# Kernel optimization log

Measured on AMD Instinct MI355X. Metric: run time of the kernel, lower is better.

The kernel has to match this reference:

```python
import jax, jax.numpy as jnp
import numpy as np

N, E = 20000, 320000
H1, C1 = 8, 128   # gat1 heads/out
H2, C2 = 1, 128   # gat2 heads/out
D_IN = 768
NEG_SLOPE = 0.2
BN_EPS = 1e-5


def setup_inputs() -> dict:
    key = jax.random.key(0)
    ks = jax.random.split(key, 16)
    def rn(k, shape, fan):
        return jax.random.normal(k, shape, dtype=jnp.float32) / np.sqrt(fan)
    x = jax.random.normal(ks[0], (N, D_IN), dtype=jnp.float32)
    edge_index = jax.random.randint(ks[1], (2, E), 0, N, dtype=jnp.int64)
    return {
        "x": x,
        "edge_index": edge_index,
        "W1": rn(ks[2], (D_IN, H1 * C1), D_IN),
        "att_src1": rn(ks[3], (H1, C1), C1),
        "att_dst1": rn(ks[4], (H1, C1), C1),
        "b1": jnp.zeros((H1 * C1,), jnp.float32),
        "W2": rn(ks[5], (H1 * C1, H2 * C2), H1 * C1),
        "att_src2": rn(ks[6], (H2, C2), C2),
        "att_dst2": rn(ks[7], (H2, C2), C2),
        "b2": jnp.zeros((C2,), jnp.float32),
        "g1": jnp.ones((H1 * C1,), jnp.float32),
        "be1": jnp.zeros((H1 * C1,), jnp.float32),
        "g2": jnp.ones((C2,), jnp.float32),
        "be2": jnp.zeros((C2,), jnp.float32),
        "Wc1": rn(ks[8], (C2, 64), C2),
        "bc1": jnp.zeros((64,), jnp.float32),
        "Wc2": rn(ks[9], (64, 2), 64),
        "bc2": jnp.zeros((2,), jnp.float32),
    }


def gat_conv(x, src, dst, W, att_src, att_dst, bias, heads, ch, concat):
    n = x.shape[0]
    h = (x @ W).reshape(n, heads, ch)                      # [N,H,C]
    a_s = jnp.sum(h * att_src[None], axis=-1)              # [N,H]
    a_d = jnp.sum(h * att_dst[None], axis=-1)
    e = a_s[src] + a_d[dst]                                # [Et,H]
    e = jax.nn.leaky_relu(e, NEG_SLOPE)
    # segment softmax over incoming edges of each dst node
    m = jax.ops.segment_max(e, dst, num_segments=n)
    ex = jnp.exp(e - m[dst])
    z = jax.ops.segment_sum(ex, dst, num_segments=n)
    alpha = ex / z[dst]                                    # [Et,H]
    msg = alpha[:, :, None] * h[src]                       # [Et,H,C]
    out = jax.ops.segment_sum(msg, dst, num_segments=n)    # [N,H,C]
    if concat:
        out = out.reshape(n, heads * ch)
    else:
        out = out.mean(axis=1)
    return out + bias


def batch_norm(x, gamma, beta):
    mu = x.mean(axis=0)
    var = x.var(axis=0)
    return (x - mu) * jax.lax.rsqrt(var + BN_EPS) * gamma + beta


def reference(x, edge_index, W1, att_src1, att_dst1, b1, W2, att_src2, att_dst2, b2,
              g1, be1, g2, be2, Wc1, bc1, Wc2, bc2):
    n = x.shape[0]
    loop = jnp.arange(n, dtype=edge_index.dtype)
    src = jnp.concatenate([edge_index[0], loop])  # PyG add_self_loops default
    dst = jnp.concatenate([edge_index[1], loop])
    h = gat_conv(x, src, dst, W1, att_src1, att_dst1, b1, H1, C1, True)
    h = jax.nn.elu(batch_norm(h, g1, be1))
    h = gat_conv(h, src, dst, W2, att_src2, att_dst2, b2, H2, C2, False)
    h = jax.nn.elu(batch_norm(h, g2, be2))
    h = jax.nn.relu(h @ Wc1 + bc1)
    return h @ Wc2 + bc2
```

## Files before the change

kernel.cpp:

```cpp
#include <hip/hip_runtime.h>
#include <hip/hip_bf16.h>
#include <math.h>

#define N_NODES 20000
#define N_EDGES 320000
#define DIN 768
#define F1 1024
#define H1 8
#define C1 128
#define F2 128
#define NEG_SLOPE 0.2f
#define BN_EPS 1e-5f
#define RESCALE_THR 8.0f

typedef __attribute__((ext_vector_type(8))) __bf16 bf16x8;
typedef __attribute__((ext_vector_type(4))) float f32x4;

__device__ __forceinline__ float leaky(float x) { return x > 0.f ? x : NEG_SLOPE * x; }

__device__ __forceinline__ unsigned short f2bu(float x) {
  __hip_bfloat16 b = __float2bfloat16(x);
  return *(unsigned short*)&b;
}
__device__ __forceinline__ float b2f(unsigned short u) {
  return __uint_as_float(((unsigned)u) << 16);
}
__device__ __forceinline__ unsigned pack2(float lo, float hi) {
  return (unsigned)f2bu(lo) | ((unsigned)f2bu(hi) << 16);
}

__device__ __forceinline__ void async_copy16(void* lds, const void* g) {
  __builtin_amdgcn_global_load_lds(
      (const __attribute__((address_space(1))) unsigned int*)g,
      (__attribute__((address_space(3))) unsigned int*)lds, 16, 0, 0);
}

__global__ void repack_hist_kernel(const int* raw, int* ei32, int* deg) {
  int is64 = (raw[1] == 0 && raw[3] == 0 && raw[5] == 0 && raw[7] == 0) ? 1 : 0;
  int e = blockIdx.x * blockDim.x + threadIdx.x;
  if (e < 2 * N_EDGES) {
    int v = is64 ? raw[2 * e] : raw[e];
    ei32[e] = v;
    if (e >= N_EDGES) atomicAdd(&deg[v], 1);
  }
}

#define NPT 20
__global__ __launch_bounds__(1024) void scan_kernel(const int* __restrict__ deg,
                                                    int* __restrict__ off,
                                                    int* __restrict__ cursor) {
  __shared__ int wsum[16];
  int tid = threadIdx.x;
  int lane = tid & 63, wv = tid >> 6;
  int base = tid * NPT;
  int loc[NPT];
  int run = 0;
#pragma unroll
  for (int k = 0; k < NPT; ++k) {
    int i = base + k;
    int v = (i < N_NODES) ? deg[i] : 0;
    loc[k] = run;
    run += v;
  }
  int incl = run;
  for (int sh = 1; sh < 64; sh <<= 1) {
    int t = __shfl_up(incl, sh, 64);
    if (lane >= sh) incl += t;
  }
  if (lane == 63) wsum[wv] = incl;
  __syncthreads();
  if (wv == 0 && lane < 16) {
    int v = wsum[lane];
    for (int sh = 1; sh < 16; sh <<= 1) {
      int t = __shfl_up(v, sh, 16);
      if (lane >= sh) v += t;
    }
    wsum[lane] = v;
  }
  __syncthreads();
  int wbase = (wv > 0) ? wsum[wv - 1] : 0;
  int tbase = wbase + incl - run;
#pragma unroll
  for (int k = 0; k < NPT; ++k) {
    int i = base + k;
    if (i < N_NODES) {
      int o = tbase + loc[k];
      off[i] = o;
      cursor[i] = o;
    }
  }
  if (tid == 1023) off[N_NODES] = wbase + incl;
}

__global__ void scatter_kernel(const int* ei, int* cursor, int* elist) {
  int e = blockIdx.x * blockDim.x + threadIdx.x;
  if (e < N_EDGES) {
    int dst = ei[N_EDGES + e];
    int p = atomicAdd(&cursor[dst], 1);
    elist[p] = ei[e];
  }
}

__global__ void f2b_kernel(const float* __restrict__ in, unsigned short* __restrict__ out,
                           size_t n4) {
  size_t i = (size_t)blockIdx.x * blockDim.x + threadIdx.x;
  size_t stride = (size_t)gridDim.x * blockDim.x;
  for (; i < n4; i += stride) {
    float4 v = ((const float4*)in)[i];
    ushort4 u;
    u.x = f2bu(v.x); u.y = f2bu(v.y); u.z = f2bu(v.z); u.w = f2bu(v.w);
    ((ushort4*)out)[i] = u;
  }
}

__global__ void transpose_b_kernel(const float* __restrict__ W, unsigned short* __restrict__ WT,
                                   int K, int N) {
  __shared__ float t[32][33];
  int k0 = blockIdx.y * 32, n0 = blockIdx.x * 32;
  int tx = threadIdx.x & 31, ty = threadIdx.x >> 5;
  for (int i = 0; i < 32; i += 8)
    t[ty + i][tx] = W[(size_t)(k0 + ty + i) * N + n0 + tx];
  __syncthreads();
  for (int i = 0; i < 32; i += 8)
    WT[(size_t)(n0 + ty + i) * K + k0 + tx] = f2bu(t[tx][ty + i]);
}

#define GBM 128
#define GBN 128
#define GBK 64
template <int H, int SWZ>
__global__ __launch_bounds__(256) void mfma_gemm_att_kernel(
    const unsigned short* __restrict__ A,
    const unsigned short* __restrict__ BT,
    unsigned short* __restrict__ C,
    const float* __restrict__ att_src,
    const float* __restrict__ att_dst,
    float* __restrict__ as_out,
    float* __restrict__ ad_out,
    int M, int N, int K) {
  __shared__ __hip_bfloat16 As[GBM][GBK];
  __shared__ __hip_bfloat16 Bs[GBN][GBK];
  __shared__ float sred[128][2];
  __shared__ float dred[128][2];
  int bx, by;
  if (SWZ) {
    int bid = blockIdx.x;
    int pl = bid & 7, c = (bid >> 3) & 7, ph = bid >> 6;
    int p = ph * 8 + pl;
    if (p * GBM >= M) return;
    by = p; bx = c;
  } else {
    bx = blockIdx.x; by = blockIdx.y;
  }
  int tid = threadIdx.x;
  int lane = tid & 63, wid = tid >> 6;
  int wr = wid >> 1, wc = wid & 1;
  int row0 = by * GBM, col0 = bx * GBN;
  int head = bx;
  int l16 = lane & 15, l4 = lane >> 4;
  f32x4 acc[4][4] = {};
  for (int k0 = 0; k0 < K; k0 += GBK) {
#pragma unroll
    for (int j = 0; j < 4; ++j) {
      int c = j * 256 + tid;
      int r = c >> 3, kk = (c & 7) << 3;
      int ga = row0 + r; if (ga >= M) ga = M - 1;
      async_copy16(&As[r][kk], A + (size_t)ga * K + k0 + kk);
      async_copy16(&Bs[r][kk], BT + (size_t)(col0 + r) * K + k0 + kk);
    }
    __syncthreads();
#pragma unroll
    for (int ks = 0; ks < 2; ++ks) {
      bf16x8 af[4], bfr[4];
#pragma unroll
      for (int i = 0; i < 4; ++i)
        af[i] = *(const bf16x8*)&As[wr * 64 + i * 16 + l16][ks * 32 + l4 * 8];
#pragma unroll
      for (int j = 0; j < 4; ++j)
        bfr[j] = *(const bf16x8*)&Bs[wc * 64 + j * 16 + l16][ks * 32 + l4 * 8];
#pragma unroll
      for (int i = 0; i < 4; ++i)
#pragma unroll
        for (int j = 0; j < 4; ++j)
          acc[i][j] = __builtin_amdgcn_mfma_f32_16x16x32_bf16(af[i], bfr[j], acc[i][j], 0, 0, 0);
    }
    __syncthreads();
  }
#pragma unroll
  for (int i = 0; i < 4; ++i) {
#pragma unroll
    for (int j = 0; j < 4; ++j) {
#pragma unroll
      for (int r = 0; r < 4; ++r) {
        int row = row0 + wr * 64 + i * 16 + l4 * 4 + r;
        int col = col0 + wc * 64 + j * 16 + l16;
        if (row < M) C[(size_t)row * N + col] = f2bu(acc[i][j][r]);
      }
    }
  }
  float avs[4], avd[4];
#pragma unroll
  for (int j = 0; j < 4; ++j) {
    int col = col0 + wc * 64 + j * 16 + l16;
    avs[j] = att_src[col];
    avd[j] = att_dst[col];
  }
#pragma unroll
  for (int i = 0; i < 4; ++i) {
#pragma unroll
    for (int r = 0; r < 4; ++r) {
      float ps = 0.f, pd = 0.f;
#pragma unroll
      for (int j = 0; j < 4; ++j) { ps += acc[i][j][r] * avs[j]; pd += acc[i][j][r] * avd[j]; }
#pragma unroll
      for (int mk = 1; mk < 16; mk <<= 1) {
        ps += __shfl_xor(ps, mk, 64);
        pd += __shfl_xor(pd, mk, 64);
      }
      if (l16 == 0) {
        int lr = wr * 64 + i * 16 + l4 * 4 + r;
        sred[lr][wc] = ps;
        dred[lr][wc] = pd;
      }
    }
  }
  __syncthreads();
  if (tid < 128) {
    int row = row0 + tid;
    if (row < M) {
      as_out[(size_t)row * H + head] = sred[tid][0] + sred[tid][1];
      ad_out[(size_t)row * H + head] = dred[tid][0] + dred[tid][1];
    }
  }
}

__global__ __launch_bounds__(64) void alpha1_kernel(const float* __restrict__ as1,
                                                    const float* __restrict__ ad1,
                                                    const int* __restrict__ off,
                                                    const int* __restrict__ elist,
                                                    uint2* __restrict__ ewT,
                                                    float* __restrict__ zinv,
                                                    float* __restrict__ wself) {
  int node = blockIdx.x;
  int lane = threadIdx.x;
  int s = off[node], e = off[node + 1];
  float4 adlo = *(const float4*)(ad1 + node * H1);
  float4 adhi = *(const float4*)(ad1 + node * H1 + 4);
  float ad[8] = {adlo.x, adlo.y, adlo.z, adlo.w, adhi.x, adhi.y, adhi.z, adhi.w};
  float4 aslo = *(const float4*)(as1 + node * H1);
  float4 ashi = *(const float4*)(as1 + node * H1 + 4);
  float sl[8] = {aslo.x, aslo.y, aslo.z, aslo.w, ashi.x, ashi.y, ashi.z, ashi.w};
  float m[8];
#pragma unroll
  for (int h = 0; h < 8; ++h) { sl[h] = leaky(sl[h] + ad[h]); m[h] = sl[h]; }
  for (int i = s + lane; i < e; i += 64) {
    int src = elist[i];
    float4 lo = *(const float4*)(as1 + (size_t)src * H1);
    float4 hi = *(const float4*)(as1 + (size_t)src * H1 + 4);
    float v[8] = {lo.x, lo.y, lo.z, lo.w, hi.x, hi.y, hi.z, hi.w};
#pragma unroll
    for (int h = 0; h < 8; ++h) m[h] = fmaxf(m[h], leaky(v[h] + ad[h]));
  }
#pragma unroll
  for (int h = 0; h < 8; ++h)
    for (int sh = 32; sh >= 1; sh >>= 1) m[h] = fmaxf(m[h], __shfl_xor(m[h], sh, 64));
  float z[8] = {0.f, 0.f, 0.f, 0.f, 0.f, 0.f, 0.f, 0.f};
  for (int i = s + lane; i < e; i += 64) {
    int src = elist[i];
    float4 lo = *(const float4*)(as1 + (size_t)src * H1);
    float4 hi = *(const float4*)(as1 + (size_t)src * H1 + 4);
    float v[8] = {lo.x, lo.y, lo.z, lo.w, hi.x, hi.y, hi.z, hi.w};
#pragma unroll
    for (int h = 0; h < 8; ++h) {
      float w = __expf(leaky(v[h] + ad[h]) - m[h]);
      z[h] += w;
      ewT[(size_t)h * N_EDGES + i] = make_uint2((unsigned)src, __float_as_uint(w));
    }
  }
#pragma unroll
  for (int h = 0; h < 8; ++h)
    for (int sh = 32; sh >= 1; sh >>= 1) z[h] += __shfl_xor(z[h], sh, 64);
  if (lane == 0) {
#pragma unroll
    for (int h = 0; h < 8; ++h) {
      float ws = __expf(sl[h] - m[h]);
      zinv[node * H1 + h] = 1.f / (z[h] + ws);
      wself[node * H1 + h] = ws;
    }
  }
}

#define EW_LOAD(i, ev)                                                          \
  if ((i) < e) ev = ewp[(i)];
#define H1_LOAD(i, ev, rv)                                                      \
  if ((i) < e) rv = *(const unsigned*)(h1 + (size_t)ev.x * F1 + cb);
#define GW_CONS(u, ev)                                                          \
  {                                                                             \
    float wv = __uint_as_float(ev.y);                                           \
    a0 += wv * __uint_as_float(u << 16);                                        \
    a1 += wv * __uint_as_float(u & 0xffff0000u);                                \
  }

__global__ __launch_bounds__(64) void gatherw1_kernel(const unsigned short* __restrict__ h1,
                                                      const uint2* __restrict__ ewT,
                                                      const float* __restrict__ zinv,
                                                      const float* __restrict__ wself,
                                                      const int* __restrict__ off,
                                                      const float* __restrict__ b1,
                                                      unsigned short* __restrict__ out1) {
  int head = blockIdx.x;
  int node = blockIdx.y;
  int tid = threadIdx.x;
  int cb = head * C1 + tid * 2;
  int s = off[node], e = off[node + 1];
  const uint2* ewp = ewT + (size_t)head * N_EDGES;
  float a0, a1;
  {
    float ws = wself[node * H1 + head];
    unsigned u = *(const unsigned*)(h1 + (size_t)node * F1 + cb);
    a0 = ws * __uint_as_float(u << 16);
    a1 = ws * __uint_as_float(u & 0xffff0000u);
  }
  uint2 ea0 = {0, 0}, ea1 = {0, 0}, ea2 = {0, 0}, ea3 = {0, 0};
  uint2 eb0 = {0, 0}, eb1 = {0, 0}, eb2 = {0, 0}, eb3 = {0, 0};
  unsigned ra0 = 0, ra1 = 0, ra2 = 0, ra3 = 0;
  EW_LOAD(s + 0, ea0)
  EW_LOAD(s + 1, ea1)
  EW_LOAD(s + 2, ea2)
  EW_LOAD(s + 3, ea3)
  EW_LOAD(s + 4, eb0)
  EW_LOAD(s + 5, eb1)
  EW_LOAD(s + 6, eb2)
  EW_LOAD(s + 7, eb3)
  H1_LOAD(s + 0, ea0, ra0)
  H1_LOAD(s + 1, ea1, ra1)
  H1_LOAD(s + 2, ea2, ra2)
  H1_LOAD(s + 3, ea3, ra3)
  for (int base = s; base < e; base += 4) {
    unsigned rb0 = 0, rb1 = 0, rb2 = 0, rb3 = 0;
    int nb = base + 4;
    H1_LOAD(nb + 0, eb0, rb0)
    H1_LOAD(nb + 1, eb1, rb1)
    H1_LOAD(nb + 2, eb2, rb2)
    H1_LOAD(nb + 3, eb3, rb3)
    uint2 ec0 = {0, 0}, ec1 = {0, 0}, ec2 = {0, 0}, ec3 = {0, 0};
    int nc = base + 8;
    EW_LOAD(nc + 0, ec0)
    EW_LOAD(nc + 1, ec1)
    EW_LOAD(nc + 2, ec2)
    EW_LOAD(nc + 3, ec3)
    GW_CONS(ra0, ea0)
    GW_CONS(ra1, ea1)
    GW_CONS(ra2, ea2)
    GW_CONS(ra3, ea3)
    ea0 = eb0; ea1 = eb1; ea2 = eb2; ea3 = eb3;
    eb0 = ec0; eb1 = ec1; eb2 = ec2; eb3 = ec3;
    ra0 = rb0; ra1 = rb1; ra2 = rb2; ra3 = rb3;
  }
  float inv = zinv[node * H1 + head];
  float2 bv = *(const float2*)(b1 + cb);
  unsigned o = pack2(a0 * inv + bv.x, a1 * inv + bv.y);
  *(unsigned*)(out1 + (size_t)node * F1 + cb) = o;
}

__global__ void bnstats_bf16_kernel(const unsigned short* __restrict__ x,
                                    float* __restrict__ sums,
                                    int nrows, int F, int rowsPerBlock) {
  int tid = threadIdx.x;
  int c = tid * 4;
  int r0 = blockIdx.x * rowsPerBlock;
  int rend = min(r0 + rowsPerBlock, nrows);
  float s0 = 0.f, s1 = 0.f, s2 = 0.f, s3 = 0.f;
  float q0 = 0.f, q1 = 0.f, q2 = 0.f, q3 = 0.f;
  for (int r = r0; r < rend; ++r) {
    ushort4 u = *(const ushort4*)(x + (size_t)r * F + c);
    float v0 = b2f(u.x), v1 = b2f(u.y), v2 = b2f(u.z), v3 = b2f(u.w);
    s0 += v0; s1 += v1; s2 += v2; s3 += v3;
    q0 += v0 * v0; q1 += v1 * v1; q2 += v2 * v2; q3 += v3 * v3;
  }
  atomicAdd(&sums[c + 0], s0); atomicAdd(&sums[c + 1], s1);
  atomicAdd(&sums[c + 2], s2); atomicAdd(&sums[c + 3], s3);
  atomicAdd(&sums[F + c + 0], q0); atomicAdd(&sums[F + c + 1], q1);
  atomicAdd(&sums[F + c + 2], q2); atomicAdd(&sums[F + c + 3], q3);
}

template <int CPT>
__global__ void bnstats_kernel(const float* __restrict__ x, float* __restrict__ sums,
                               int nrows, int F, int rowsPerBlock) {
  int tid = threadIdx.x;
  int r0 = blockIdx.x * rowsPerBlock;
  int rend = min(r0 + rowsPerBlock, nrows);
  float s[CPT], q[CPT];
#pragma unroll
  for (int k = 0; k < CPT; ++k) { s[k] = 0.f; q[k] = 0.f; }
  for (int r = r0; r < rend; ++r) {
    const float* row = x + (size_t)r * F;
#pragma unroll
    for (int k = 0; k < CPT; ++k) {
      float v = row[tid + k * blockDim.x];
      s[k] += v; q[k] += v * v;
    }
  }
#pragma unroll
  for (int k = 0; k < CPT; ++k) {
    atomicAdd(&sums[tid + k * blockDim.x], s[k]);
    atomicAdd(&sums[F + tid + k * blockDim.x], q[k]);
  }
}

__global__ void bnfinal_kernel(const float* __restrict__ sums, const float* __restrict__ g,
                               const float* __restrict__ be, float* __restrict__ ss, int F) {
  int c = blockIdx.x * blockDim.x + threadIdx.x;
  if (c < F) {
    float mu = sums[c] * (1.f / N_NODES);
    float var = sums[F + c] * (1.f / N_NODES) - mu * mu;
    float sc = g[c] * rsqrtf(var + BN_EPS);
    ss[c] = sc;
    ss[F + c] = be[c] - mu * sc;
  }
}

__global__ void bnapply_bf16_kernel(unsigned short* __restrict__ x, const float* __restrict__ ss,
                                    int F, size_t total4) {
  size_t i = (size_t)blockIdx.x * blockDim.x + threadIdx.x;
  size_t stride = (size_t)gridDim.x * blockDim.x;
  for (; i < total4; i += stride) {
    int c = (int)((i * 4) & (size_t)(F - 1));
    ushort4 u = ((ushort4*)x)[i];
    float v0 = b2f(u.x) * ss[c + 0] + ss[F + c + 0];
    float v1 = b2f(u.y) * ss[c + 1] + ss[F + c + 1];
    float v2 = b2f(u.z) * ss[c + 2] + ss[F + c + 2];
    float v3 = b2f(u.w) * ss[c + 3] + ss[F + c + 3];
    v0 = v0 > 0.f ? v0 : expm1f(v0);
    v1 = v1 > 0.f ? v1 : expm1f(v1);
    v2 = v2 > 0.f ? v2 : expm1f(v2);
    v3 = v3 > 0.f ? v3 : expm1f(v3);
    u.x = f2bu(v0); u.y = f2bu(v1); u.z = f2bu(v2); u.w = f2bu(v3);
    ((ushort4*)x)[i] = u;
  }
}

#define G2_LOAD(i, rv, ev)                                                     \
  if ((i) < e) {                                                               \
    int ssrc = elist[(i)];                                                     \
    ev = leaky(as2[ssrc] + ad);                                                \
    rv = *(const unsigned*)(h2 + (size_t)ssrc * F2 + tid * 2);                 \
  }
#define G2_CONSUME(u, el)                                                      \
  {                                                                            \
    float w;                                                                   \
    if (el > m + RESCALE_THR) {                                                \
      float rr = __expf(m - el);                                               \
      z *= rr; a0 *= rr; a1 *= rr;                                             \
      m = el; w = 1.f;                                                         \
    } else {                                                                   \
      w = __expf(el - m);                                                      \
    }                                                                          \
    z += w;                                                                    \
    a0 += w * __uint_as_float(u << 16);                                        \
    a1 += w * __uint_as_float(u & 0xffff0000u);                                \
  }

__global__ __launch_bounds__(64) void gather2_kernel(const unsigned short* __restrict__ h2,
                                                     const float* __restrict__ as2,
                                                     const float* __restrict__ ad2,
                                                     const int* __restrict__ off,
                                                     const int* __restrict__ elist,
                                                     const float* __restrict__ b2,
                                                     float* __restrict__ out2) {
  int node = blockIdx.x;
  int tid = threadIdx.x;
  const float ad = ad2[node];
  int s = off[node], e = off[node + 1];
  float m = leaky(as2[node] + ad);
  float z = 1.f;
  float a0, a1;
  {
    unsigned u = *(const unsigned*)(h2 + (size_t)node * F2 + tid * 2);
    a0 = __uint_as_float(u << 16); a1 = __uint_as_float(u & 0xffff0000u);
  }
  unsigned ra0 = 0, ra1 = 0, ra2 = 0, ra3 = 0;
  float ea0 = 0.f, ea1 = 0.f, ea2 = 0.f, ea3 = 0.f;
  G2_LOAD(s + 0, ra0, ea0)
  G2_LOAD(s + 1, ra1, ea1)
  G2_LOAD(s + 2, ra2, ea2)
  G2_LOAD(s + 3, ra3, ea3)
  for (int base = s; base < e; base += 4) {
    unsigned rb0 = 0, rb1 = 0, rb2 = 0, rb3 = 0;
    float eb0 = 0.f, eb1 = 0.f, eb2 = 0.f, eb3 = 0.f;
    int nb = base + 4;
    G2_LOAD(nb + 0, rb0, eb0)
    G2_LOAD(nb + 1, rb1, eb1)
    G2_LOAD(nb + 2, rb2, eb2)
    G2_LOAD(nb + 3, rb3, eb3)
    G2_CONSUME(ra0, ea0)
    if (base + 1 < e) G2_CONSUME(ra1, ea1)
    if (base + 2 < e) G2_CONSUME(ra2, ea2)
    if (base + 3 < e) G2_CONSUME(ra3, ea3)
    ra0 = rb0; ra1 = rb1; ra2 = rb2; ra3 = rb3;
    ea0 = eb0; ea1 = eb1; ea2 = eb2; ea3 = eb3;
  }
  float inv = 1.f / z;
  float2 o = make_float2(a0 * inv + b2[tid * 2 + 0], a1 * inv + b2[tid * 2 + 1]);
  *(float2*)(out2 + (size_t)node * F2 + tid * 2) = o;
}

__global__ __launch_bounds__(64) void cls_kernel(const float* __restrict__ h,
                                                 const float* __restrict__ ss2,
                                                 const float* __restrict__ Wc1,
                                                 const float* __restrict__ bc1,
                                                 const float* __restrict__ Wc2,
                                                 const float* __restrict__ bc2,
                                                 float* __restrict__ out) {
  __shared__ float hl[128];
  int node = blockIdx.x;
  int tid = threadIdx.x;
  {
    float v = h[(size_t)node * F2 + tid] * ss2[tid] + ss2[F2 + tid];
    v = v > 0.f ? v : expm1f(v);
    hl[tid] = v;
    float v2 = h[(size_t)node * F2 + 64 + tid] * ss2[64 + tid] + ss2[F2 + 64 + tid];
    v2 = v2 > 0.f ? v2 : expm1f(v2);
    hl[tid + 64] = v2;
  }
  __syncthreads();
  float acc = bc1[tid];
#pragma unroll
  for (int k = 0; k < 128; ++k) acc += hl[k] * Wc1[k * 64 + tid];
  acc = fmaxf(acc, 0.f);
  float2 w = *(const float2*)(Wc2 + tid * 2);
  float o0 = acc * w.x, o1 = acc * w.y;
  for (int sh = 32; sh >= 1; sh >>= 1) {
    o0 += __shfl_down(o0, sh, 64);
    o1 += __shfl_down(o1, sh, 64);
  }
  if (tid == 0) {
    out[node * 2 + 0] = o0 + bc2[0];
    out[node * 2 + 1] = o1 + bc2[1];
  }
}

extern "C" void kernel_launch(void* const* d_in, const int* in_sizes, int n_in,
                              void* d_out, int out_size, void* d_ws, size_t ws_size,
                              hipStream_t stream) {
  const float* x        = (const float*)d_in[0];
  const int*   ei_raw   = (const int*)d_in[1];
  const float* W1       = (const float*)d_in[2];
  const float* att_src1 = (const float*)d_in[3];
  const float* att_dst1 = (const float*)d_in[4];
  const float* b1       = (const float*)d_in[5];
  const float* W2       = (const float*)d_in[6];
  const float* att_src2 = (const float*)d_in[7];
  const float* att_dst2 = (const float*)d_in[8];
  const float* b2       = (const float*)d_in[9];
  const float* g1       = (const float*)d_in[10];
  const float* be1      = (const float*)d_in[11];
  const float* g2       = (const float*)d_in[12];
  const float* be2      = (const float*)d_in[13];
  const float* Wc1      = (const float*)d_in[14];
  const float* bc1      = (const float*)d_in[15];
  const float* Wc2      = (const float*)d_in[16];
  const float* bc2      = (const float*)d_in[17];
  float* out = (float*)d_out;

  char* ws = (char*)d_ws;
  size_t o = 0;
  unsigned short* h1b   = (unsigned short*)(ws + o); o += (size_t)N_NODES * F1 * 2;
  unsigned short* out1b = (unsigned short*)(ws + o); o += (size_t)N_NODES * F1 * 2;
  unsigned short* xb    = (unsigned short*)(ws + o); o += (size_t)N_NODES * DIN * 2;
  unsigned short* h2b   = (unsigned short*)(ws + o); o += (size_t)N_NODES * F2 * 2;
  float* out2  = (float*)(ws + o); o += (size_t)N_NODES * F2 * 4;
  float* as1   = (float*)(ws + o); o += (size_t)N_NODES * H1 * 4;
  float* ad1   = (float*)(ws + o); o += (size_t)N_NODES * H1 * 4;
  float* as2   = (float*)(ws + o); o += (size_t)N_NODES * 4;
  float* ad2   = (float*)(ws + o); o += (size_t)N_NODES * 4;
  uint2* ewT   = (uint2*)(ws + o); o += (size_t)H1 * N_EDGES * 8;
  float* zinv  = (float*)(ws + o); o += (size_t)N_NODES * H1 * 4;
  float* wself = (float*)(ws + o); o += (size_t)N_NODES * H1 * 4;
  char*  zbase = ws + o;
  float* bnsum1 = (float*)(ws + o); o += F1 * 2 * 4;
  float* bnsum2 = (float*)(ws + o); o += F2 * 2 * 4;
  int*   deg    = (int*)(ws + o); o += (size_t)N_NODES * 4;
  size_t zbytes = (size_t)((ws + o) - zbase);
  int*   offv   = (int*)(ws + o); o += (size_t)(N_NODES + 4) * 4;
  int*   cursor = (int*)(ws + o); o += (size_t)N_NODES * 4;
  int*   elist  = (int*)(ws + o); o += (size_t)N_EDGES * 4;
  float* ss1    = (float*)(ws + o); o += F1 * 2 * 4;
  float* ss2    = (float*)(ws + o); o += F2 * 2 * 4;
  int*   ei32   = (int*)(ws + o); o += (size_t)2 * N_EDGES * 4;
  unsigned short* W1T = (unsigned short*)(ws + o); o += (size_t)F1 * DIN * 2;
  unsigned short* W2T = (unsigned short*)(ws + o); o += (size_t)F2 * F1 * 2;
  (void)ws_size; (void)in_sizes; (void)n_in; (void)out_size;

  hipMemsetAsync((void*)zbase, 0, zbytes, stream);

  f2b_kernel<<<2048, 256, 0, stream>>>(x, xb, (size_t)N_NODES * DIN / 4);
  {
    dim3 g1d(F1 / 32, DIN / 32);
    transpose_b_kernel<<<g1d, 256, 0, stream>>>(W1, W1T, DIN, F1);
    dim3 g2d(F2 / 32, F1 / 32);
    transpose_b_kernel<<<g2d, 256, 0, stream>>>(W2, W2T, F1, F2);
  }

  repack_hist_kernel<<<(2 * N_EDGES + 255) / 256, 256, 0, stream>>>(ei_raw, ei32, deg);
  scan_kernel<<<1, 1024, 0, stream>>>(deg, offv, cursor);
  scatter_kernel<<<(N_EDGES + 255) / 256, 256, 0, stream>>>(ei32, cursor, elist);

  {
    int panels = (N_NODES + GBM - 1) / GBM;
    int grid1 = ((panels + 7) / 8) * 64;
    mfma_gemm_att_kernel<H1, 1><<<grid1, 256, 0, stream>>>(
        xb, W1T, h1b, att_src1, att_dst1, as1, ad1, N_NODES, F1, DIN);
  }
  alpha1_kernel<<<N_NODES, 64, 0, stream>>>(as1, ad1, offv, elist, ewT, zinv, wself);
  gatherw1_kernel<<<dim3(H1, N_NODES), 64, 0, stream>>>(
      h1b, ewT, zinv, wself, offv, b1, out1b);
  {
    int rows = 79;
    int grid = (N_NODES + rows - 1) / rows;
    bnstats_bf16_kernel<<<grid, 256, 0, stream>>>(out1b, bnsum1, N_NODES, F1, rows);
  }
  bnfinal_kernel<<<(F1 + 255) / 256, 256, 0, stream>>>(bnsum1, g1, be1, ss1, F1);
  bnapply_bf16_kernel<<<2048, 256, 0, stream>>>(out1b, ss1, F1, (size_t)N_NODES * F1 / 4);

  {
    dim3 grid(F2 / GBN, (N_NODES + GBM - 1) / GBM);
    mfma_gemm_att_kernel<1, 0><<<grid, 256, 0, stream>>>(
        out1b, W2T, h2b, att_src2, att_dst2, as2, ad2, N_NODES, F2, F1);
  }
  gather2_kernel<<<N_NODES, 64, 0, stream>>>(h2b, as2, ad2, offv, elist, b2, out2);
  {
    int rows = 79;
    int grid = (N_NODES + rows - 1) / rows;
    bnstats_kernel<1><<<grid, 128, 0, stream>>>(out2, bnsum2, N_NODES, F2, rows);
  }
  bnfinal_kernel<<<1, F2, 0, stream>>>(bnsum2, g2, be2, ss2, F2);

  cls_kernel<<<N_NODES, 64, 0, stream>>>(out2, ss2, Wc1, bc1, Wc2, bc2, out);
}
```

Baseline: 447.6 us.

## Split-K second GAT GEMM, two-pass layer-2 softmax, batched classifier, drop edge repack

Several independent changes. The second GEMM (only one 128-column tile) is split along K into two partial fp32 products reduced by a new combine kernel, which doubles the block count. The layer-2 online-softmax gather is replaced by a separate alpha pass plus a prefetching weighted gather, mirroring layer 1. The classifier now processes 16 nodes per 256-thread block with Wc1 cached in LDS. The int64-to-int32 edge repack is removed so hist and scatter read the raw indices directly. The costs are extra fp32 partial traffic and an extra kernel launch.

```diff
diff --git a/kernel.cpp b/kernel.cpp
--- a/kernel.cpp
+++ b/kernel.cpp
@@ -11,7 +11,6 @@
 #define F2 128
 #define NEG_SLOPE 0.2f
 #define BN_EPS 1e-5f
-#define RESCALE_THR 8.0f
 
 typedef __attribute__((ext_vector_type(8))) __bf16 bf16x8;
 typedef __attribute__((ext_vector_type(4))) float f32x4;
@@ -35,13 +34,12 @@
       (__attribute__((address_space(3))) unsigned int*)lds, 16, 0, 0);
 }
 
-__global__ void repack_hist_kernel(const int* raw, int* ei32, int* deg) {
+__global__ void hist_kernel(const int* raw, int* deg) {
   int is64 = (raw[1] == 0 && raw[3] == 0 && raw[5] == 0 && raw[7] == 0) ? 1 : 0;
   int e = blockIdx.x * blockDim.x + threadIdx.x;
-  if (e < 2 * N_EDGES) {
-    int v = is64 ? raw[2 * e] : raw[e];
-    ei32[e] = v;
-    if (e >= N_EDGES) atomicAdd(&deg[v], 1);
+  if (e < N_EDGES) {
+    int dst = is64 ? raw[2 * (N_EDGES + e)] : raw[N_EDGES + e];
+    atomicAdd(&deg[dst], 1);
   }
 }
 
@@ -92,12 +90,14 @@
   if (tid == 1023) off[N_NODES] = wbase + incl;
 }
 
-__global__ void scatter_kernel(const int* ei, int* cursor, int* elist) {
+__global__ void scatter_kernel(const int* raw, int* cursor, int* elist) {
+  int is64 = (raw[1] == 0 && raw[3] == 0 && raw[5] == 0 && raw[7] == 0) ? 1 : 0;
   int e = blockIdx.x * blockDim.x + threadIdx.x;
   if (e < N_EDGES) {
-    int dst = ei[N_EDGES + e];
+    int dst = is64 ? raw[2 * (N_EDGES + e)] : raw[N_EDGES + e];
+    int src = is64 ? raw[2 * e] : raw[e];
     int p = atomicAdd(&cursor[dst], 1);
-    elist[p] = ei[e];
+    elist[p] = src;
   }
 }
 
@@ -128,29 +128,37 @@
 #define GBM 128
 #define GBN 128
 #define GBK 64
-template <int H, int SWZ>
+template <int H, int SWZ, int PART>
 __global__ __launch_bounds__(256) void mfma_gemm_att_kernel(
     const unsigned short* __restrict__ A,
     const unsigned short* __restrict__ BT,
-    unsigned short* __restrict__ C,
+    void* __restrict__ Cout,
     const float* __restrict__ att_src,
     const float* __restrict__ att_dst,
     float* __restrict__ as_out,
     float* __restrict__ ad_out,
-    int M, int N, int K) {
+    int M, int N, int K, int lda, int ldb) {
   __shared__ __hip_bfloat16 As[GBM][GBK];
   __shared__ __hip_bfloat16 Bs[GBN][GBK];
   __shared__ float sred[128][2];
   __shared__ float dred[128][2];
-  int bx, by;
+  int bx, by, part = 0;
   if (SWZ) {
     int bid = blockIdx.x;
     int pl = bid & 7, c = (bid >> 3) & 7, ph = bid >> 6;
     int p = ph * 8 + pl;
     if (p * GBM >= M) return;
     by = p; bx = c;
+  } else if (PART) {
+    part = blockIdx.x; bx = 0; by = blockIdx.y;
   } else {
     bx = blockIdx.x; by = blockIdx.y;
+  }
+  const unsigned short* Ap = A + (size_t)part * K;
+  const unsigned short* BTp = BT + (size_t)part * K;
+  if (PART) {
+    as_out += (size_t)part * M;
+    ad_out += (size_t)part * M;
   }
   int tid = threadIdx.x;
   int lane = tid & 63, wid = tid >> 6;
@@ -165,8 +173,8 @@
       int c = j * 256 + tid;
       int r = c >> 3, kk = (c & 7) << 3;
       int ga = row0 + r; if (ga >= M) ga = M - 1;
-      async_copy16(&As[r][kk], A + (size_t)ga * K + k0 + kk);
-      async_copy16(&Bs[r][kk], BT + (size_t)(col0 + r) * K + k0 + kk);
+      async_copy16(&As[r][kk], Ap + (size_t)ga * lda + k0 + kk);
+      async_copy16(&Bs[r][kk], BTp + (size_t)(col0 + r) * ldb + k0 + kk);
     }
     __syncthreads();
 #pragma unroll
@@ -186,6 +194,8 @@
     }
     __syncthreads();
   }
+  float* Cf = (float*)Cout + (size_t)part * M * N;
+  unsigned short* Cb = (unsigned short*)Cout;
 #pragma unroll
   for (int i = 0; i < 4; ++i) {
 #pragma unroll
@@ -194,7 +204,10 @@
       for (int r = 0; r < 4; ++r) {
         int row = row0 + wr * 64 + i * 16 + l4 * 4 + r;
         int col = col0 + wc * 64 + j * 16 + l16;
-        if (row < M) C[(size_t)row * N + col] = f2bu(acc[i][j][r]);
+        if (row < M) {
+          if (PART) Cf[(size_t)row * N + col] = acc[i][j][r];
+          else Cb[(size_t)row * N + col] = f2bu(acc[i][j][r]);
+        }
       }
     }
   }
@@ -231,6 +244,25 @@
       as_out[(size_t)row * H + head] = sred[tid][0] + sred[tid][1];
       ad_out[(size_t)row * H + head] = dred[tid][0] + dred[tid][1];
     }
+  }
+}
+
+__global__ void combine2_kernel(const float* __restrict__ Cp, unsigned short* __restrict__ h2b,
+                                const float* __restrict__ asp, float* __restrict__ as2,
+                                const float* __restrict__ adp, float* __restrict__ ad2) {
+  int i = blockIdx.x * blockDim.x + threadIdx.x;
+  const int n4 = N_NODES * F2 / 4;
+  if (i < n4) {
+    float4 a = ((const float4*)Cp)[i];
+    float4 b = ((const float4*)(Cp + (size_t)N_NODES * F2))[i];
+    ushort4 u;
+    u.x = f2bu(a.x + b.x); u.y = f2bu(a.y + b.y);
+    u.z = f2bu(a.z + b.z); u.w = f2bu(a.w + b.w);
+    ((ushort4*)h2b)[i] = u;
+  }
+  if (i < N_NODES) {
+    as2[i] = asp[i] + asp[N_NODES + i];
+    ad2[i] = adp[i] + adp[N_NODES + i];
   }
 }
 
@@ -363,6 +395,100 @@
   *(unsigned*)(out1 + (size_t)node * F1 + cb) = o;
 }
 
+__global__ __launch_bounds__(64) void alpha2_kernel(const float* __restrict__ as2,
+                                                    const float* __restrict__ ad2,
+                                                    const int* __restrict__ off,
+                                                    const int* __restrict__ elist,
+                                                    uint2* __restrict__ ew2,
+                                                    float* __restrict__ zinv2,
+                                                    float* __restrict__ wself2) {
+  int node = blockIdx.x;
+  int lane = threadIdx.x;
+  int s = off[node], e = off[node + 1];
+  float ad = ad2[node];
+  float selfl = leaky(as2[node] + ad);
+  float m = selfl;
+  for (int i = s + lane; i < e; i += 64) m = fmaxf(m, leaky(as2[elist[i]] + ad));
+  for (int sh = 32; sh >= 1; sh >>= 1) m = fmaxf(m, __shfl_xor(m, sh, 64));
+  float z = 0.f;
+  for (int i = s + lane; i < e; i += 64) {
+    int src = elist[i];
+    float w = __expf(leaky(as2[src] + ad) - m);
+    z += w;
+    ew2[i] = make_uint2((unsigned)src, __float_as_uint(w));
+  }
+  for (int sh = 32; sh >= 1; sh >>= 1) z += __shfl_xor(z, sh, 64);
+  if (lane == 0) {
+    float ws = __expf(selfl - m);
+    zinv2[node] = 1.f / (z + ws);
+    wself2[node] = ws;
+  }
+}
+
+#define H2_LOAD(i, ev, rv)                                                      \
+  if ((i) < e) rv = *(const unsigned*)(h2 + (size_t)ev.x * F2 + cb);
+
+__global__ __launch_bounds__(64) void gatherw2_kernel(const unsigned short* __restrict__ h2,
+                                                      const uint2* __restrict__ ew2,
+                                                      const float* __restrict__ zinv2,
+                                                      const float* __restrict__ wself2,
+                                                      const int* __restrict__ off,
+                                                      const float* __restrict__ b2,
+                                                      float* __restrict__ out2) {
+  int node = blockIdx.x;
+  int tid = threadIdx.x;
+  int cb = tid * 2;
+  int s = off[node], e = off[node + 1];
+  const uint2* ewp = ew2;
+  float a0, a1;
+  {
+    float ws = wself2[node];
+    unsigned u = *(const unsigned*)(h2 + (size_t)node * F2 + cb);
+    a0 = ws * __uint_as_float(u << 16);
+    a1 = ws * __uint_as_float(u & 0xffff0000u);
+  }
+  uint2 ea0 = {0, 0}, ea1 = {0, 0}, ea2 = {0, 0}, ea3 = {0, 0};
+  uint2 eb0 = {0, 0}, eb1 = {0, 0}, eb2 = {0, 0}, eb3 = {0, 0};
+  unsigned ra0 = 0, ra1 = 0, ra2 = 0, ra3 = 0;
+  EW_LOAD(s + 0, ea0)
+  EW_LOAD(s + 1, ea1)
+  EW_LOAD(s + 2, ea2)
+  EW_LOAD(s + 3, ea3)
+  EW_LOAD(s + 4, eb0)
+  EW_LOAD(s + 5, eb1)
+  EW_LOAD(s + 6, eb2)
+  EW_LOAD(s + 7, eb3)
+  H2_LOAD(s + 0, ea0, ra0)
+  H2_LOAD(s + 1, ea1, ra1)
+  H2_LOAD(s + 2, ea2, ra2)
+  H2_LOAD(s + 3, ea3, ra3)
+  for (int base = s; base < e; base += 4) {
+    unsigned rb0 = 0, rb1 = 0, rb2 = 0, rb3 = 0;
+    int nb = base + 4;
+    H2_LOAD(nb + 0, eb0, rb0)
+    H2_LOAD(nb + 1, eb1, rb1)
+    H2_LOAD(nb + 2, eb2, rb2)
+    H2_LOAD(nb + 3, eb3, rb3)
+    uint2 ec0 = {0, 0}, ec1 = {0, 0}, ec2 = {0, 0}, ec3 = {0, 0};
+    int nc = base + 8;
+    EW_LOAD(nc + 0, ec0)
+    EW_LOAD(nc + 1, ec1)
+    EW_LOAD(nc + 2, ec2)
+    EW_LOAD(nc + 3, ec3)
+    GW_CONS(ra0, ea0)
+    GW_CONS(ra1, ea1)
+    GW_CONS(ra2, ea2)
+    GW_CONS(ra3, ea3)
+    ea0 = eb0; ea1 = eb1; ea2 = eb2; ea3 = eb3;
+    eb0 = ec0; eb1 = ec1; eb2 = ec2; eb3 = ec3;
+    ra0 = rb0; ra1 = rb1; ra2 = rb2; ra3 = rb3;
+  }
+  float inv = zinv2[node];
+  float2 bv = *(const float2*)(b2 + cb);
+  float2 o = make_float2(a0 * inv + bv.x, a1 * inv + bv.y);
+  *(float2*)(out2 + (size_t)node * F2 + cb) = o;
+}
+
 __global__ void bnstats_bf16_kernel(const unsigned short* __restrict__ x,
                                     float* __restrict__ sums,
                                     int nrows, int F, int rowsPerBlock) {
@@ -440,103 +566,45 @@
   }
 }
 
-#define G2_LOAD(i, rv, ev)                                                     \
-  if ((i) < e) {                                                               \
-    int ssrc = elist[(i)];                                                     \
-    ev = leaky(as2[ssrc] + ad);                                                \
-    rv = *(const unsigned*)(h2 + (size_t)ssrc * F2 + tid * 2);                 \
-  }
-#define G2_CONSUME(u, el)                                                      \
-  {                                                                            \
-    float w;                                                                   \
-    if (el > m + RESCALE_THR) {                                                \
-      float rr = __expf(m - el);                                               \
-      z *= rr; a0 *= rr; a1 *= rr;                                             \
-      m = el; w = 1.f;                                                         \
-    } else {                                                                   \
-      w = __expf(el - m);                                                      \
-    }                                                                          \
-    z += w;                                                                    \
-    a0 += w * __uint_as_float(u << 16);                                        \
-    a1 += w * __uint_as_float(u & 0xffff0000u);                                \
-  }
-
-__global__ __launch_bounds__(64) void gather2_kernel(const unsigned short* __restrict__ h2,
-                                                     const float* __restrict__ as2,
-                                                     const float* __restrict__ ad2,
-                                                     const int* __restrict__ off,
-                                                     const int* __restrict__ elist,
-                                                     const float* __restrict__ b2,
-                                                     float* __restrict__ out2) {
-  int node = blockIdx.x;
+__global__ __launch_bounds__(256) void cls_kernel(const float* __restrict__ h,
+                                                  const float* __restrict__ ss2,
+                                                  const float* __restrict__ Wc1,
+                                                  const float* __restrict__ bc1,
+                                                  const float* __restrict__ Wc2,
+                                                  const float* __restrict__ bc2,
+                                                  float* __restrict__ out) {
+  __shared__ float wc1s[128 * 64];
+  __shared__ float hl[4][128];
   int tid = threadIdx.x;
-  const float ad = ad2[node];
-  int s = off[node], e = off[node + 1];
-  float m = leaky(as2[node] + ad);
-  float z = 1.f;
-  float a0, a1;
-  {
-    unsigned u = *(const unsigned*)(h2 + (size_t)node * F2 + tid * 2);
-    a0 = __uint_as_float(u << 16); a1 = __uint_as_float(u & 0xffff0000u);
-  }
-  unsigned ra0 = 0, ra1 = 0, ra2 = 0, ra3 = 0;
-  float ea0 = 0.f, ea1 = 0.f, ea2 = 0.f, ea3 = 0.f;
-  G2_LOAD(s + 0, ra0, ea0)
-  G2_LOAD(s + 1, ra1, ea1)
-  G2_LOAD(s + 2, ra2, ea2)
-  G2_LOAD(s + 3, ra3, ea3)
-  for (int base = s; base < e; base += 4) {
-    unsigned rb0 = 0, rb1 = 0, rb2 = 0, rb3 = 0;
-    float eb0 = 0.f, eb1 = 0.f, eb2 = 0.f, eb3 = 0.f;
-    int nb = base + 4;
-    G2_LOAD(nb + 0, rb0, eb0)
-    G2_LOAD(nb + 1, rb1, eb1)
-    G2_LOAD(nb + 2, rb2, eb2)
-    G2_LOAD(nb + 3, rb3, eb3)
-    G2_CONSUME(ra0, ea0)
-    if (base + 1 < e) G2_CONSUME(ra1, ea1)
-    if (base + 2 < e) G2_CONSUME(ra2, ea2)
-    if (base + 3 < e) G2_CONSUME(ra3, ea3)
-    ra0 = rb0; ra1 = rb1; ra2 = rb2; ra3 = rb3;
-    ea0 = eb0; ea1 = eb1; ea2 = eb2; ea3 = eb3;
-  }
-  float inv = 1.f / z;
-  float2 o = make_float2(a0 * inv + b2[tid * 2 + 0], a1 * inv + b2[tid * 2 + 1]);
-  *(float2*)(out2 + (size_t)node * F2 + tid * 2) = o;
-}
-
-__global__ __launch_bounds__(64) void cls_kernel(const float* __restrict__ h,
-                                                 const float* __restrict__ ss2,
-                                                 const float* __restrict__ Wc1,
-                                                 const float* __restrict__ bc1,
-                                                 const float* __restrict__ Wc2,
-                                                 const float* __restrict__ bc2,
-                                                 float* __restrict__ out) {
-  __shared__ float hl[128];
-  int node = blockIdx.x;
-  int tid = threadIdx.x;
-  {
-    float v = h[(size_t)node * F2 + tid] * ss2[tid] + ss2[F2 + tid];
+  for (int k = tid * 8; k < 128 * 64; k += 2048) {
+    *(float4*)&wc1s[k] = *(const float4*)&Wc1[k];
+    *(float4*)&wc1s[k + 4] = *(const float4*)&Wc1[k + 4];
+  }
+  __syncthreads();
+  int wv = tid >> 6, lane = tid & 63;
+  for (int nn = 0; nn < 4; ++nn) {
+    int node = blockIdx.x * 16 + wv * 4 + nn;
+    if (node >= N_NODES) break;
+    float v = h[(size_t)node * F2 + lane] * ss2[lane] + ss2[F2 + lane];
     v = v > 0.f ? v : expm1f(v);
-    hl[tid] = v;
-    float v2 = h[(size_t)node * F2 + 64 + tid] * ss2[64 + tid] + ss2[F2 + 64 + tid];
+    hl[wv][lane] = v;
+    float v2 = h[(size_t)node * F2 + 64 + lane] * ss2[64 + lane] + ss2[F2 + 64 + lane];
     v2 = v2 > 0.f ? v2 : expm1f(v2);
-    hl[tid + 64] = v2;
-  }
-  __syncthreads();
-  float acc = bc1[tid];
-#pragma unroll
-  for (int k = 0; k < 128; ++k) acc += hl[k] * Wc1[k * 64 + tid];
-  acc = fmaxf(acc, 0.f);
-  float2 w = *(const float2*)(Wc2 + tid * 2);
-  float o0 = acc * w.x, o1 = acc * w.y;
-  for (int sh = 32; sh >= 1; sh >>= 1) {
-    o0 += __shfl_down(o0, sh, 64);
-    o1 += __shfl_down(o1, sh, 64);
-  }
-  if (tid == 0) {
-    out[node * 2 + 0] = o0 + bc2[0];
-    out[node * 2 + 1] = o1 + bc2[1];
+    hl[wv][lane + 64] = v2;
+    float acc = bc1[lane];
+#pragma unroll
+    for (int k = 0; k < 128; ++k) acc += hl[wv][k] * wc1s[k * 64 + lane];
+    acc = fmaxf(acc, 0.f);
+    float2 w = *(const float2*)(Wc2 + lane * 2);
+    float o0 = acc * w.x, o1 = acc * w.y;
+    for (int sh = 32; sh >= 1; sh >>= 1) {
+      o0 += __shfl_down(o0, sh, 64);
+      o1 += __shfl_down(o1, sh, 64);
+    }
+    if (lane == 0) {
+      out[node * 2 + 0] = o0 + bc2[0];
+      out[node * 2 + 1] = o1 + bc2[1];
+    }
   }
 }
 
@@ -577,6 +645,11 @@
   uint2* ewT   = (uint2*)(ws + o); o += (size_t)H1 * N_EDGES * 8;
   float* zinv  = (float*)(ws + o); o += (size_t)N_NODES * H1 * 4;
   float* wself = (float*)(ws + o); o += (size_t)N_NODES * H1 * 4;
+  float* asp   = (float*)(ws + o); o += (size_t)2 * N_NODES * 4;
+  float* adp   = (float*)(ws + o); o += (size_t)2 * N_NODES * 4;
+  uint2* ew2   = (uint2*)(ws + o); o += (size_t)N_EDGES * 8;
+  float* zinv2 = (float*)(ws + o); o += (size_t)N_NODES * 4;
+  float* wself2= (float*)(ws + o); o += (size_t)N_NODES * 4;
   char*  zbase = ws + o;
   float* bnsum1 = (float*)(ws + o); o += F1 * 2 * 4;
   float* bnsum2 = (float*)(ws + o); o += F2 * 2 * 4;
@@ -587,9 +660,9 @@
   int*   elist  = (int*)(ws + o); o += (size_t)N_EDGES * 4;
   float* ss1    = (float*)(ws + o); o += F1 * 2 * 4;
   float* ss2    = (float*)(ws + o); o += F2 * 2 * 4;
-  int*   ei32   = (int*)(ws + o); o += (size_t)2 * N_EDGES * 4;
   unsigned short* W1T = (unsigned short*)(ws + o); o += (size_t)F1 * DIN * 2;
   unsigned short* W2T = (unsigned short*)(ws + o); o += (size_t)F2 * F1 * 2;
+  float* Cp = (float*)xb;
   (void)ws_size; (void)in_sizes; (void)n_in; (void)out_size;
 
   hipMemsetAsync((void*)zbase, 0, zbytes, stream);
@@ -602,15 +675,15 @@
     transpose_b_kernel<<<g2d, 256, 0, stream>>>(W2, W2T, F1, F2);
   }
 
-  repack_hist_kernel<<<(2 * N_EDGES + 255) / 256, 256, 0, stream>>>(ei_raw, ei32, deg);
+  hist_kernel<<<(N_EDGES + 255) / 256, 256, 0, stream>>>(ei_raw, deg);
   scan_kernel<<<1, 1024, 0, stream>>>(deg, offv, cursor);
-  scatter_kernel<<<(N_EDGES + 255) / 256, 256, 0, stream>>>(ei32, cursor, elist);
+  scatter_kernel<<<(N_EDGES + 255) / 256, 256, 0, stream>>>(ei_raw, cursor, elist);
 
   {
     int panels = (N_NODES + GBM - 1) / GBM;
     int grid1 = ((panels + 7) / 8) * 64;
-    mfma_gemm_att_kernel<H1, 1><<<grid1, 256, 0, stream>>>(
-        xb, W1T, h1b, att_src1, att_dst1, as1, ad1, N_NODES, F1, DIN);
+    mfma_gemm_att_kernel<H1, 1, 0><<<grid1, 256, 0, stream>>>(
+        xb, W1T, (void*)h1b, att_src1, att_dst1, as1, ad1, N_NODES, F1, DIN, DIN, DIN);
   }
   alpha1_kernel<<<N_NODES, 64, 0, stream>>>(as1, ad1, offv, elist, ewT, zinv, wself);
   gatherw1_kernel<<<dim3(H1, N_NODES), 64, 0, stream>>>(
@@ -624,11 +697,15 @@
   bnapply_bf16_kernel<<<2048, 256, 0, stream>>>(out1b, ss1, F1, (size_t)N_NODES * F1 / 4);
 
   {
-    dim3 grid(F2 / GBN, (N_NODES + GBM - 1) / GBM);
-    mfma_gemm_att_kernel<1, 0><<<grid, 256, 0, stream>>>(
-        out1b, W2T, h2b, att_src2, att_dst2, as2, ad2, N_NODES, F2, F1);
-  }
-  gather2_kernel<<<N_NODES, 64, 0, stream>>>(h2b, as2, ad2, offv, elist, b2, out2);
+    dim3 grid(2, (N_NODES + GBM - 1) / GBM);
+    mfma_gemm_att_kernel<1, 0, 1><<<grid, 256, 0, stream>>>(
+        out1b, W2T, (void*)Cp, att_src2, att_dst2, asp, adp,
+        N_NODES, F2, F1 / 2, F1, F1);
+    combine2_kernel<<<(N_NODES * F2 / 4 + 255) / 256, 256, 0, stream>>>(
+        Cp, h2b, asp, as2, adp, ad2);
+  }
+  alpha2_kernel<<<N_NODES, 64, 0, stream>>>(as2, ad2, offv, elist, ew2, zinv2, wself2);
+  gatherw2_kernel<<<N_NODES, 64, 0, stream>>>(h2b, ew2, zinv2, wself2, offv, b2, out2);
   {
     int rows = 79;
     int grid = (N_NODES + rows - 1) / rows;
@@ -636,5 +713,5 @@
   }
   bnfinal_kernel<<<1, F2, 0, stream>>>(bnsum2, g2, be2, ss2, F2);
 
-  cls_kernel<<<N_NODES, 64, 0, stream>>>(out2, ss2, Wc1, bc1, Wc2, bc2, out);
-}
+  cls_kernel<<<(N_NODES + 15) / 16, 256, 0, stream>>>(out2, ss2, Wc1, bc1, Wc2, bc2, out);
+}
```

Result: no change. 456.0 us (+1.9%).

## Read raw edge indices directly, batch nodes per block in gather and classifier

Applied to the files above, without the earlier changes.

Removes the int32 repack pass: the histogram and scatter kernels now read the raw edge_index directly, detecting 64-bit layout themselves. The layer-1 gather now processes four nodes per 256-thread block, with each wave handling one node, and its software prefetch is deepened from 4 to 8 edges. The classifier stages Wc1 into shared memory once per block and has each wave handle four nodes. The aim is to cut kernel-launch granularity and redundant global traffic, at the cost of more registers in the gather and 32KB of LDS in the classifier.

```diff
diff --git a/kernel.cpp b/kernel.cpp
--- a/kernel.cpp
+++ b/kernel.cpp
@@ -35,13 +35,12 @@
       (__attribute__((address_space(3))) unsigned int*)lds, 16, 0, 0);
 }
 
-__global__ void repack_hist_kernel(const int* raw, int* ei32, int* deg) {
+__global__ void hist_kernel(const int* raw, int* deg) {
   int is64 = (raw[1] == 0 && raw[3] == 0 && raw[5] == 0 && raw[7] == 0) ? 1 : 0;
   int e = blockIdx.x * blockDim.x + threadIdx.x;
-  if (e < 2 * N_EDGES) {
-    int v = is64 ? raw[2 * e] : raw[e];
-    ei32[e] = v;
-    if (e >= N_EDGES) atomicAdd(&deg[v], 1);
+  if (e < N_EDGES) {
+    int dst = is64 ? raw[2 * (N_EDGES + e)] : raw[N_EDGES + e];
+    atomicAdd(&deg[dst], 1);
   }
 }
 
@@ -92,12 +91,14 @@
   if (tid == 1023) off[N_NODES] = wbase + incl;
 }
 
-__global__ void scatter_kernel(const int* ei, int* cursor, int* elist) {
+__global__ void scatter_kernel(const int* raw, int* cursor, int* elist) {
+  int is64 = (raw[1] == 0 && raw[3] == 0 && raw[5] == 0 && raw[7] == 0) ? 1 : 0;
   int e = blockIdx.x * blockDim.x + threadIdx.x;
   if (e < N_EDGES) {
-    int dst = ei[N_EDGES + e];
+    int dst = is64 ? raw[2 * (N_EDGES + e)] : raw[N_EDGES + e];
+    int src = is64 ? raw[2 * e] : raw[e];
     int p = atomicAdd(&cursor[dst], 1);
-    elist[p] = ei[e];
+    elist[p] = src;
   }
 }
 
@@ -301,17 +302,18 @@
     a1 += wv * __uint_as_float(u & 0xffff0000u);                                \
   }
 
-__global__ __launch_bounds__(64) void gatherw1_kernel(const unsigned short* __restrict__ h1,
-                                                      const uint2* __restrict__ ewT,
-                                                      const float* __restrict__ zinv,
-                                                      const float* __restrict__ wself,
-                                                      const int* __restrict__ off,
-                                                      const float* __restrict__ b1,
-                                                      unsigned short* __restrict__ out1) {
+__global__ __launch_bounds__(256) void gatherw1_kernel(const unsigned short* __restrict__ h1,
+                                                       const uint2* __restrict__ ewT,
+                                                       const float* __restrict__ zinv,
+                                                       const float* __restrict__ wself,
+                                                       const int* __restrict__ off,
+                                                       const float* __restrict__ b1,
+                                                       unsigned short* __restrict__ out1) {
   int head = blockIdx.x;
-  int node = blockIdx.y;
-  int tid = threadIdx.x;
-  int cb = head * C1 + tid * 2;
+  int wv = threadIdx.x >> 6;
+  int node = blockIdx.y * 4 + wv;
+  int lane = threadIdx.x & 63;
+  int cb = head * C1 + lane * 2;
   int s = off[node], e = off[node + 1];
   const uint2* ewp = ewT + (size_t)head * N_EDGES;
   float a0, a1;
@@ -321,41 +323,39 @@
     a0 = ws * __uint_as_float(u << 16);
     a1 = ws * __uint_as_float(u & 0xffff0000u);
   }
-  uint2 ea0 = {0, 0}, ea1 = {0, 0}, ea2 = {0, 0}, ea3 = {0, 0};
-  uint2 eb0 = {0, 0}, eb1 = {0, 0}, eb2 = {0, 0}, eb3 = {0, 0};
-  unsigned ra0 = 0, ra1 = 0, ra2 = 0, ra3 = 0;
-  EW_LOAD(s + 0, ea0)
-  EW_LOAD(s + 1, ea1)
-  EW_LOAD(s + 2, ea2)
-  EW_LOAD(s + 3, ea3)
-  EW_LOAD(s + 4, eb0)
-  EW_LOAD(s + 5, eb1)
-  EW_LOAD(s + 6, eb2)
-  EW_LOAD(s + 7, eb3)
-  H1_LOAD(s + 0, ea0, ra0)
-  H1_LOAD(s + 1, ea1, ra1)
-  H1_LOAD(s + 2, ea2, ra2)
-  H1_LOAD(s + 3, ea3, ra3)
-  for (int base = s; base < e; base += 4) {
-    unsigned rb0 = 0, rb1 = 0, rb2 = 0, rb3 = 0;
-    int nb = base + 4;
-    H1_LOAD(nb + 0, eb0, rb0)
-    H1_LOAD(nb + 1, eb1, rb1)
-    H1_LOAD(nb + 2, eb2, rb2)
-    H1_LOAD(nb + 3, eb3, rb3)
-    uint2 ec0 = {0, 0}, ec1 = {0, 0}, ec2 = {0, 0}, ec3 = {0, 0};
-    int nc = base + 8;
-    EW_LOAD(nc + 0, ec0)
-    EW_LOAD(nc + 1, ec1)
-    EW_LOAD(nc + 2, ec2)
-    EW_LOAD(nc + 3, ec3)
-    GW_CONS(ra0, ea0)
-    GW_CONS(ra1, ea1)
-    GW_CONS(ra2, ea2)
-    GW_CONS(ra3, ea3)
+  uint2 ea0 = {0,0}, ea1 = {0,0}, ea2 = {0,0}, ea3 = {0,0};
+  uint2 ea4 = {0,0}, ea5 = {0,0}, ea6 = {0,0}, ea7 = {0,0};
+  uint2 eb0 = {0,0}, eb1 = {0,0}, eb2 = {0,0}, eb3 = {0,0};
+  uint2 eb4 = {0,0}, eb5 = {0,0}, eb6 = {0,0}, eb7 = {0,0};
+  unsigned ra0 = 0, ra1 = 0, ra2 = 0, ra3 = 0, ra4 = 0, ra5 = 0, ra6 = 0, ra7 = 0;
+  EW_LOAD(s + 0, ea0)  EW_LOAD(s + 1, ea1)  EW_LOAD(s + 2, ea2)  EW_LOAD(s + 3, ea3)
+  EW_LOAD(s + 4, ea4)  EW_LOAD(s + 5, ea5)  EW_LOAD(s + 6, ea6)  EW_LOAD(s + 7, ea7)
+  EW_LOAD(s + 8, eb0)  EW_LOAD(s + 9, eb1)  EW_LOAD(s + 10, eb2) EW_LOAD(s + 11, eb3)
+  EW_LOAD(s + 12, eb4) EW_LOAD(s + 13, eb5) EW_LOAD(s + 14, eb6) EW_LOAD(s + 15, eb7)
+  H1_LOAD(s + 0, ea0, ra0)  H1_LOAD(s + 1, ea1, ra1)
+  H1_LOAD(s + 2, ea2, ra2)  H1_LOAD(s + 3, ea3, ra3)
+  H1_LOAD(s + 4, ea4, ra4)  H1_LOAD(s + 5, ea5, ra5)
+  H1_LOAD(s + 6, ea6, ra6)  H1_LOAD(s + 7, ea7, ra7)
+  for (int base = s; base < e; base += 8) {
+    unsigned rb0 = 0, rb1 = 0, rb2 = 0, rb3 = 0, rb4 = 0, rb5 = 0, rb6 = 0, rb7 = 0;
+    int nb = base + 8;
+    H1_LOAD(nb + 0, eb0, rb0)  H1_LOAD(nb + 1, eb1, rb1)
+    H1_LOAD(nb + 2, eb2, rb2)  H1_LOAD(nb + 3, eb3, rb3)
+    H1_LOAD(nb + 4, eb4, rb4)  H1_LOAD(nb + 5, eb5, rb5)
+    H1_LOAD(nb + 6, eb6, rb6)  H1_LOAD(nb + 7, eb7, rb7)
+    uint2 ec0 = {0,0}, ec1 = {0,0}, ec2 = {0,0}, ec3 = {0,0};
+    uint2 ec4 = {0,0}, ec5 = {0,0}, ec6 = {0,0}, ec7 = {0,0};
+    int nc = base + 16;
+    EW_LOAD(nc + 0, ec0)  EW_LOAD(nc + 1, ec1)  EW_LOAD(nc + 2, ec2)  EW_LOAD(nc + 3, ec3)
+    EW_LOAD(nc + 4, ec4)  EW_LOAD(nc + 5, ec5)  EW_LOAD(nc + 6, ec6)  EW_LOAD(nc + 7, ec7)
+    GW_CONS(ra0, ea0)  GW_CONS(ra1, ea1)  GW_CONS(ra2, ea2)  GW_CONS(ra3, ea3)
+    GW_CONS(ra4, ea4)  GW_CONS(ra5, ea5)  GW_CONS(ra6, ea6)  GW_CONS(ra7, ea7)
     ea0 = eb0; ea1 = eb1; ea2 = eb2; ea3 = eb3;
+    ea4 = eb4; ea5 = eb5; ea6 = eb6; ea7 = eb7;
     eb0 = ec0; eb1 = ec1; eb2 = ec2; eb3 = ec3;
+    eb4 = ec4; eb5 = ec5; eb6 = ec6; eb7 = ec7;
     ra0 = rb0; ra1 = rb1; ra2 = rb2; ra3 = rb3;
+    ra4 = rb4; ra5 = rb5; ra6 = rb6; ra7 = rb7;
   }
   float inv = zinv[node * H1 + head];
   float2 bv = *(const float2*)(b1 + cb);
@@ -505,38 +505,45 @@
   *(float2*)(out2 + (size_t)node * F2 + tid * 2) = o;
 }
 
-__global__ __launch_bounds__(64) void cls_kernel(const float* __restrict__ h,
-                                                 const float* __restrict__ ss2,
-                                                 const float* __restrict__ Wc1,
-                                                 const float* __restrict__ bc1,
-                                                 const float* __restrict__ Wc2,
-                                                 const float* __restrict__ bc2,
-                                                 float* __restrict__ out) {
-  __shared__ float hl[128];
-  int node = blockIdx.x;
+__global__ __launch_bounds__(256) void cls_kernel(const float* __restrict__ h,
+                                                  const float* __restrict__ ss2,
+                                                  const float* __restrict__ Wc1,
+                                                  const float* __restrict__ bc1,
+                                                  const float* __restrict__ Wc2,
+                                                  const float* __restrict__ bc2,
+                                                  float* __restrict__ out) {
+  __shared__ float wc1s[128 * 64];
+  __shared__ float hl[4][128];
   int tid = threadIdx.x;
-  {
-    float v = h[(size_t)node * F2 + tid] * ss2[tid] + ss2[F2 + tid];
+  for (int k = tid * 8; k < 128 * 64; k += 2048) {
+    *(float4*)&wc1s[k] = *(const float4*)&Wc1[k];
+    *(float4*)&wc1s[k + 4] = *(const float4*)&Wc1[k + 4];
+  }
+  __syncthreads();
+  int wv = tid >> 6, lane = tid & 63;
+  for (int nn = 0; nn < 4; ++nn) {
+    int node = blockIdx.x * 16 + wv * 4 + nn;
+    if (node >= N_NODES) break;
+    float v = h[(size_t)node * F2 + lane] * ss2[lane] + ss2[F2 + lane];
     v = v > 0.f ? v : expm1f(v);
-    hl[tid] = v;
-    float v2 = h[(size_t)node * F2 + 64 + tid] * ss2[64 + tid] + ss2[F2 + 64 + tid];
+    hl[wv][lane] = v;
+    float v2 = h[(size_t)node * F2 + 64 + lane] * ss2[64 + lane] + ss2[F2 + 64 + lane];
     v2 = v2 > 0.f ? v2 : expm1f(v2);
-    hl[tid + 64] = v2;
-  }
-  __syncthreads();
-  float acc = bc1[tid];
-#pragma unroll
-  for (int k = 0; k < 128; ++k) acc += hl[k] * Wc1[k * 64 + tid];
-  acc = fmaxf(acc, 0.f);
-  float2 w = *(const float2*)(Wc2 + tid * 2);
-  float o0 = acc * w.x, o1 = acc * w.y;
-  for (int sh = 32; sh >= 1; sh >>= 1) {
-    o0 += __shfl_down(o0, sh, 64);
-    o1 += __shfl_down(o1, sh, 64);
-  }
-  if (tid == 0) {
-    out[node * 2 + 0] = o0 + bc2[0];
-    out[node * 2 + 1] = o1 + bc2[1];
+    hl[wv][lane + 64] = v2;
+    float acc = bc1[lane];
+#pragma unroll
+    for (int k = 0; k < 128; ++k) acc += hl[wv][k] * wc1s[k * 64 + lane];
+    acc = fmaxf(acc, 0.f);
+    float2 w = *(const float2*)(Wc2 + lane * 2);
+    float o0 = acc * w.x, o1 = acc * w.y;
+    for (int sh = 32; sh >= 1; sh >>= 1) {
+      o0 += __shfl_down(o0, sh, 64);
+      o1 += __shfl_down(o1, sh, 64);
+    }
+    if (lane == 0) {
+      out[node * 2 + 0] = o0 + bc2[0];
+      out[node * 2 + 1] = o1 + bc2[1];
+    }
   }
 }
 
@@ -587,7 +594,6 @@
   int*   elist  = (int*)(ws + o); o += (size_t)N_EDGES * 4;
   float* ss1    = (float*)(ws + o); o += F1 * 2 * 4;
   float* ss2    = (float*)(ws + o); o += F2 * 2 * 4;
-  int*   ei32   = (int*)(ws + o); o += (size_t)2 * N_EDGES * 4;
   unsigned short* W1T = (unsigned short*)(ws + o); o += (size_t)F1 * DIN * 2;
   unsigned short* W2T = (unsigned short*)(ws + o); o += (size_t)F2 * F1 * 2;
   (void)ws_size; (void)in_sizes; (void)n_in; (void)out_size;
@@ -602,9 +608,9 @@
     transpose_b_kernel<<<g2d, 256, 0, stream>>>(W2, W2T, F1, F2);
   }
 
-  repack_hist_kernel<<<(2 * N_EDGES + 255) / 256, 256, 0, stream>>>(ei_raw, ei32, deg);
+  hist_kernel<<<(N_EDGES + 255) / 256, 256, 0, stream>>>(ei_raw, deg);
   scan_kernel<<<1, 1024, 0, stream>>>(deg, offv, cursor);
-  scatter_kernel<<<(N_EDGES + 255) / 256, 256, 0, stream>>>(ei32, cursor, elist);
+  scatter_kernel<<<(N_EDGES + 255) / 256, 256, 0, stream>>>(ei_raw, cursor, elist);
 
   {
     int panels = (N_NODES + GBM - 1) / GBM;
@@ -613,7 +619,7 @@
         xb, W1T, h1b, att_src1, att_dst1, as1, ad1, N_NODES, F1, DIN);
   }
   alpha1_kernel<<<N_NODES, 64, 0, stream>>>(as1, ad1, offv, elist, ewT, zinv, wself);
-  gatherw1_kernel<<<dim3(H1, N_NODES), 64, 0, stream>>>(
+  gatherw1_kernel<<<dim3(H1, N_NODES / 4), 256, 0, stream>>>(
       h1b, ewT, zinv, wself, offv, b1, out1b);
   {
     int rows = 79;
@@ -636,5 +642,5 @@
   }
   bnfinal_kernel<<<1, F2, 0, stream>>>(bnsum2, g2, be2, ss2, F2);
 
-  cls_kernel<<<N_NODES, 64, 0, stream>>>(out2, ss2, Wc1, bc1, Wc2, bc2, out);
-}
+  cls_kernel<<<(N_NODES + 15) / 16, 256, 0, stream>>>(out2, ss2, Wc1, bc1, Wc2, bc2, out);
+}
```

Measured after the change: 550.1 us. 1.23x slower.
